# Kernel optimization log

Measured on AMD Instinct MI355X. Metric: run time of the kernel, lower is better.

The kernel has to match this reference:

```python
import jax, jax.numpy as jnp
import numpy as np

B, S, D, H = 2, 2048, 1024, 16
DK = D // H


def setup_inputs() -> dict:
    key = jax.random.key(0)
    ks = jax.random.split(key, 12)
    init = lambda k, shp: (jax.random.normal(k, shp, dtype=jnp.float32) * 0.02)
    return {
        'query': jax.random.normal(ks[0], (B, S, D), dtype=jnp.float32),
        'key_in': jax.random.normal(ks[1], (B, S, D), dtype=jnp.float32),
        'value': jax.random.normal(ks[2], (B, S, D), dtype=jnp.float32),
        'w_q': init(ks[3], (D, D)), 'b_q': jnp.zeros((D,), jnp.float32),
        'w_k': init(ks[4], (D, D)), 'b_k': jnp.zeros((D,), jnp.float32),
        'w_v': init(ks[5], (D, D)), 'b_v': jnp.zeros((D,), jnp.float32),
        'w_o': init(ks[6], (D, D)), 'b_o': jnp.zeros((D,), jnp.float32),
        'fuzzy_centers': jax.random.normal(ks[7], (H, 3), dtype=jnp.float32),
        'fuzzy_widths': jnp.ones((H, 3), jnp.float32),
        'temperature': jnp.ones((1,), jnp.float32),
    }


def reference(query, key_in, value, w_q, b_q, w_k, b_k, w_v, b_v, w_o, b_o,
              fuzzy_centers, fuzzy_widths, temperature):
    b, s, d = query.shape
    h, dk = H, DK
    proj = lambda x, w, bias: x @ w.T + bias
    # [b,s,d] -> [b,h,s,dk]
    Q = proj(query, w_q, b_q).reshape(b, s, h, dk).transpose(0, 2, 1, 3)
    K = proj(key_in, w_k, b_k).reshape(b, s, h, dk).transpose(0, 2, 1, 3)
    V = proj(value, w_v, b_v).reshape(b, s, h, dk).transpose(0, 2, 1, 3)
    scores = jnp.einsum('bhsd,bhtd->bhst', Q, K) / np.sqrt(dk).astype(np.float32)
    # Faithful to torch: every (head,func) gaussian is applied to ALL heads' scores,
    # so each score gets sum of h*3 memberships, divided by 3.
    c = fuzzy_centers.reshape(-1)
    w = fuzzy_widths.reshape(-1)
    fz = jnp.zeros_like(scores)
    for i in range(h * 3):  # small fixed loop over membership functions
        fz = fz + jnp.exp(-(scores - c[i]) ** 2 / (2.0 * w[i] ** 2))
    fz = (fz / 3.0) / temperature[0]
    attn = jax.nn.softmax(fz, axis=-1)
    attended = jnp.einsum('bhst,bhtd->bhsd', attn, V)
    attended = attended.transpose(0, 2, 1, 3).reshape(b, s, d)
    return attended @ w_o.T + b_o
```

## Files before the change

### kernel.cpp

```cpp
#include <hip/hip_runtime.h>
#include <hip/hip_bf16.h>


#define S_LEN 2048
#define DMODEL 1024
#define NHEAD 16
#define DKH 64
#define NLUT 2048
#define LUT_MIN (-10.0f)
#define LUT_MAX (10.0f)

typedef __attribute__((ext_vector_type(8))) short bfx8;
typedef __attribute__((ext_vector_type(4))) float fx4;
typedef __attribute__((ext_vector_type(16))) float fx16;
typedef __attribute__((ext_vector_type(4))) unsigned ux4;

__device__ __forceinline__ short f2bf(float x) {
    unsigned u = __builtin_bit_cast(unsigned, x);
    u = (u + 0x7fffu + ((u >> 16) & 1u)) >> 16;
    return (short)u;
}

__device__ __forceinline__ unsigned cvt_pk_bf16(float lo, float hi) {
    unsigned r;
    asm("v_cvt_pk_bf16_f32 %0, %1, %2" : "=v"(r) : "v"(lo), "v"(hi));
    return r;
}

__device__ __forceinline__ void plane_swap(unsigned& a, unsigned& b) {
    asm volatile("v_permlane32_swap_b32 %0, %1" : "+v"(a), "+v"(b));
}

__device__ __forceinline__ void stage8_f32(const float* __restrict__ src, short* dst) {
    float4 a = *(const float4*)(src);
    float4 b = *(const float4*)(src + 4);
    bfx8 r;
    r[0] = f2bf(a.x); r[1] = f2bf(a.y); r[2] = f2bf(a.z); r[3] = f2bf(a.w);
    r[4] = f2bf(b.x); r[5] = f2bf(b.y); r[6] = f2bf(b.z); r[7] = f2bf(b.w);
    *(bfx8*)dst = r;
}

__device__ __forceinline__ void gload_lds16(const void* g, void* l) {
    __builtin_amdgcn_global_load_lds(
        (const __attribute__((address_space(1))) unsigned int*)g,
        (__attribute__((address_space(3))) unsigned int*)l, 16, 0, 0);
}

__device__ void lut_body(const float* __restrict__ centers, const float* __restrict__ widths,
                         const float* __restrict__ temp, float2* __restrict__ lutf) {
    __shared__ float fzb[NLUT];
    __shared__ float red[256];
    __shared__ float cs[48], wsb[48];
    int tid = threadIdx.x;
    if (tid < 48) { cs[tid] = centers[tid]; wsb[tid] = widths[tid]; }
    __syncthreads();
    float invT = 1.0f / temp[0];
    const float step = (LUT_MAX - LUT_MIN) / (float)(NLUT - 1);
    float lmax = -1e30f;
    for (int i = tid; i < NLUT; i += 256) {
        float s = LUT_MIN + step * (float)i;
        float fz = 0.0f;
        #pragma unroll 1
        for (int j = 0; j < 48; j++) {
            float d = s - cs[j];
            float w = wsb[j];
            fz += expf(-(d * d) / (2.0f * w * w));
        }
        fz = fz * (1.0f / 3.0f) * invT;
        fzb[i] = fz;
        lmax = fmaxf(lmax, fz);
    }
    red[tid] = lmax;
    __syncthreads();
    for (int off = 128; off > 0; off >>= 1) {
        if (tid < off) red[tid] = fmaxf(red[tid], red[tid + off]);
        __syncthreads();
    }
    float m = red[0];
    __syncthreads();
    for (int i = tid; i < NLUT; i += 256) fzb[i] = expf(fzb[i] - m);
    __syncthreads();
    for (int i = tid; i < NLUT; i += 256) {
        float g0 = fzb[i];
        float g1 = fzb[(i + 1 < NLUT) ? i + 1 : NLUT - 1];
        lutf[i] = make_float2(g0, g1 - g0);
    }
}

__global__ void build_lut_pk(const float* centers, const float* widths,
                             const float* temp, float2* lutf) {
    lut_body(centers, widths, temp, lutf);
}

__global__ void cast_bf16(const float* __restrict__ src, short* __restrict__ dst, int n8) {
    int i = blockIdx.x * 256 + threadIdx.x;
    if (i < n8) stage8_f32(src + (size_t)i * 8, dst + (size_t)i * 8);
}

__global__ void prep_all(const float* q, const float* kin, const float* v,
        const float* wq, const float* wk, const float* wv, const float* wo,
        short* xq, short* xk, short* xv,
        short* bwq, short* bwk, short* bwv, short* bwo,
        const float* centers, const float* widths, const float* temp,
        float2* lutf) {
    int bid = blockIdx.x;
    if (bid >= 8192) {
        lut_body(centers, widths, temp, lutf);
        return;
    }
    const float* src; short* dst; int blk;
    if (bid < 6144) {
        int y = bid >> 11; blk = bid & 2047;
        src = (y == 0) ? q : (y == 1) ? kin : v;
        dst = (y == 0) ? xq : (y == 1) ? xk : xv;
    } else {
        int y = (bid - 6144) >> 9; blk = (bid - 6144) & 511;
        src = (y == 0) ? wq : (y == 1) ? wk : (y == 2) ? wv : wo;
        dst = (y == 0) ? bwq : (y == 1) ? bwk : (y == 2) ? bwv : bwo;
    }
    size_t i = (size_t)blk * 256 + threadIdx.x;
    stage8_f32(src + i * 8, (short*)dst + i * 8);
}

struct GemmJob {
    const short* A; const short* W; const float* bias;
    short* obf; float* of32; int mode; float scale;
};

__global__ __launch_bounds__(256, 3) void gemm128(GemmJob j0, GemmJob j1, GemmJob j2) {
    __shared__ __align__(16) short As[2][128 * 32];
    __shared__ __align__(16) short Bs[2][128 * 32];
    GemmJob jb = (blockIdx.z == 0) ? j0 : (blockIdx.z == 1) ? j1 : j2;
    int tid = threadIdx.x, wave = tid >> 6, lane = tid & 63, quad = lane >> 4, l15 = lane & 15;
    int m0 = blockIdx.y * 128, n0 = blockIdx.x * 128;
    int wm = (wave >> 1) * 64, wn = (wave & 1) * 64;

    fx4 acc[4][4];
    #pragma unroll
    for (int i = 0; i < 4; i++)
        #pragma unroll
        for (int j = 0; j < 4; j++)
            #pragma unroll
            for (int r = 0; r < 4; r++) acc[i][j][r] = 0.0f;

    int fc = (quad ^ ((l15 >> 1) & 3)) * 8;

    int srow[2], sgc[2];
    #pragma unroll
    for (int r = 0; r < 2; r++) {
        int slot = r * 256 + wave * 64 + lane;
        srow[r] = slot >> 2;
        sgc[r] = (slot & 3) ^ ((srow[r] >> 1) & 3);
    }

    auto stage = [&](int k0, int buf) {
        #pragma unroll
        for (int r = 0; r < 2; r++) {
            gload_lds16(jb.A + (size_t)(m0 + srow[r]) * DMODEL + k0 + sgc[r] * 8,
                        &As[buf][(r * 256 + wave * 64) * 8]);
            gload_lds16(jb.W + (size_t)(n0 + srow[r]) * DMODEL + k0 + sgc[r] * 8,
                        &Bs[buf][(r * 256 + wave * 64) * 8]);
        }
    };

    stage(0, 0);
    __syncthreads();
    int buf = 0;
    for (int k0 = 0; k0 < DMODEL; k0 += 32) {
        if (k0 + 32 < DMODEL) stage(k0 + 32, buf ^ 1);
        bfx8 af[4], bfr[4];
        #pragma unroll
        for (int i = 0; i < 4; i++) af[i] = *(const bfx8*)(&As[buf][(wm + i * 16 + l15) * 32 + fc]);
        #pragma unroll
        for (int j = 0; j < 4; j++) bfr[j] = *(const bfx8*)(&Bs[buf][(wn + j * 16 + l15) * 32 + fc]);
        #pragma unroll
        for (int i = 0; i < 4; i++)
            #pragma unroll
            for (int j = 0; j < 4; j++)
                acc[i][j] = __builtin_amdgcn_mfma_f32_16x16x32_bf16(af[i], bfr[j], acc[i][j], 0, 0, 0);
        __syncthreads();
        buf ^= 1;
    }

    #pragma unroll
    for (int j = 0; j < 4; j++) {
        int n = n0 + wn + j * 16 + l15;
        float bv = jb.bias[n];
        #pragma unroll
        for (int i = 0; i < 4; i++) {
            #pragma unroll
            for (int r = 0; r < 4; r++) {
                int m = m0 + wm + i * 16 + quad * 4 + r;
                float v = (acc[i][j][r] + bv) * jb.scale;
                if (jb.mode == 0) {
                    int b = m >> 11, s = m & 2047, h = n >> 6, dk = n & 63;
                    jb.obf[(((size_t)(b * NHEAD + h)) * S_LEN + s) * DKH + dk] = f2bf(v);
                } else if (jb.mode == 1) {
                    int b = m >> 11, s = m & 2047, h = n >> 6, dk = n & 63;
                    jb.obf[(((size_t)(b * NHEAD + h)) * DKH + dk) * S_LEN + s] = f2bf(v);
                } else {
                    jb.of32[(size_t)m * DMODEL + n] = v;
                }
            }
        }
    }
}

__global__ __launch_bounds__(256, 4) void flash_fuzzy(const short* __restrict__ Qb,
        const short* __restrict__ Kb, const short* __restrict__ VTb,
        const float2* __restrict__ lutg, short* __restrict__ AO) {
    __shared__ __align__(16) short Ks[64 * 64];
    __shared__ __align__(16) short Vs[64 * 64];
    __shared__ __align__(16) float2 lutf[NLUT];

    int tid = threadIdx.x, wave = tid >> 6, lane = tid & 63;
    int l31 = lane & 31, hi = lane >> 5;
    int wq = wave >> 1, st = wave & 1;
    int q0 = blockIdx.x * 64, bh = blockIdx.y;
    const short* Qp = Qb + (size_t)bh * S_LEN * DKH;
    const short* Kp = Kb + (size_t)bh * S_LEN * DKH;
    const short* Vp = VTb + (size_t)bh * DKH * S_LEN;

    #pragma unroll
    for (int i = tid; i < NLUT / 2; i += 256)
        ((float4*)lutf)[i] = ((const float4*)lutg)[i];

    bfx8 aq[4];
    #pragma unroll
    for (int ks = 0; ks < 4; ks++)
        aq[ks] = *(const bfx8*)(Qp + (size_t)(q0 + wq * 32 + l31) * DKH + ks * 16 + hi * 8);

    bfx8 ones;
    #pragma unroll
    for (int i = 0; i < 8; i++) ones[i] = (short)0x3F80;

    fx16 oacc[2];
    fx16 dacc;
    #pragma unroll
    for (int r = 0; r < 16; r++) dacc[r] = 0.0f;
    #pragma unroll
    for (int dt = 0; dt < 2; dt++)
        #pragma unroll
        for (int r = 0; r < 16; r++) oacc[dt][r] = 0.0f;

    const float invh = (float)(NLUT - 1) / (LUT_MAX - LUT_MIN);
    const float xoff = -LUT_MIN * invh;

    int srow[2], sgc[2];
    #pragma unroll
    for (int r = 0; r < 2; r++) {
        int slot = (wave * 2 + r) * 64 + lane;
        srow[r] = slot >> 3;
        sgc[r] = (slot & 7) ^ (srow[r] & 7);
    }

    for (int t0 = 0; t0 < S_LEN; t0 += 64) {
        __syncthreads();
        #pragma unroll
        for (int r = 0; r < 2; r++) {
            gload_lds16(Kp + (size_t)(t0 + srow[r]) * DKH + sgc[r] * 8,
                        &Ks[((wave * 2 + r) * 64) * 8]);
            gload_lds16(Vp + (size_t)srow[r] * S_LEN + t0 + sgc[r] * 8,
                        &Vs[((wave * 2 + r) * 64) * 8]);
        }
        __syncthreads();

        fx16 sac;
        #pragma unroll
        for (int r = 0; r < 16; r++) sac[r] = 0.0f;
        {
            int row = st * 32 + l31;
            #pragma unroll
            for (int ks = 0; ks < 4; ks++) {
                bfx8 kf = *(const bfx8*)(&Ks[row * 64 + (((ks * 2 + hi) ^ (row & 7)) * 8)]);
                sac = __builtin_amdgcn_mfma_f32_32x32x16_bf16(kf, aq[ks], sac, 0, 0, 0);
            }
        }

        unsigned w[8];
        #pragma unroll
        for (int t = 0; t < 8; t++) {
            float pv[2];
            #pragma unroll
            for (int u = 0; u < 2; u++) {
                float s = sac[t * 2 + u];
                float x = fmaf(s, invh, xoff);
                x = __builtin_amdgcn_fmed3f(x, 0.0f, (float)(NLUT - 1));
                int j = (int)x;
                float f = x - floorf(x);
                float2 pr = lutf[j];
                pv[u] = fmaf(f, pr.y, pr.x);
            }
            w[t] = cvt_pk_bf16(pv[0], pv[1]);
        }

        plane_swap(w[0], w[2]); plane_swap(w[1], w[3]);
        plane_swap(w[4], w[6]); plane_swap(w[5], w[7]);
        ux4 b0v = {w[0], w[1], w[2], w[3]};
        ux4 b1v = {w[4], w[5], w[6], w[7]};
        bfx8 pb0 = __builtin_bit_cast(bfx8, b0v);
        bfx8 pb1 = __builtin_bit_cast(bfx8, b1v);

        #pragma unroll
        for (int dt = 0; dt < 2; dt++) {
            int row = dt * 32 + l31;
            bfx8 v0f = *(const bfx8*)(&Vs[row * 64 + (((st * 4 + 0 + hi) ^ (row & 7)) * 8)]);
            bfx8 v1f = *(const bfx8*)(&Vs[row * 64 + (((st * 4 + 2 + hi) ^ (row & 7)) * 8)]);
            oacc[dt] = __builtin_amdgcn_mfma_f32_32x32x16_bf16(v0f, pb0, oacc[dt], 0, 0, 0);
            oacc[dt] = __builtin_amdgcn_mfma_f32_32x32x16_bf16(v1f, pb1, oacc[dt], 0, 0, 0);
        }
        dacc = __builtin_amdgcn_mfma_f32_32x32x16_bf16(ones, pb0, dacc, 0, 0, 0);
        dacc = __builtin_amdgcn_mfma_f32_32x32x16_bf16(ones, pb1, dacc, 0, 0, 0);
    }

    float den = dacc[0];

    __syncthreads();
    float* obuf = (wq == 0) ? (float*)Ks : (float*)Vs;
    float* dbuf = (float*)lutf;
    if (st == 1) {
        #pragma unroll
        for (int dt = 0; dt < 2; dt++)
            #pragma unroll
            for (int r = 0; r < 16; r++)
                obuf[(dt * 16 + r) * 64 + lane] = oacc[dt][r];
        dbuf[wq * 64 + lane] = den;
    }
    __syncthreads();
    if (st == 0) {
        float dtot = den + dbuf[wq * 64 + lane];
        int b = bh >> 4, h = bh & 15;
        #pragma unroll
        for (int dt = 0; dt < 2; dt++) {
            #pragma unroll
            for (int r = 0; r < 16; r++) {
                float o = oacc[dt][r] + obuf[(dt * 16 + r) * 64 + lane];
                int dk = dt * 32 + (r & 3) + 8 * (r >> 2) + 4 * hi;
                int q = q0 + wq * 32 + l31;
                AO[((size_t)(b * S_LEN + q)) * DMODEL + h * DKH + dk] = f2bf(o / dtot);
            }
        }
    }
}

extern "C" void kernel_launch(void* const* d_in, const int* in_sizes, int n_in,
                              void* d_out, int out_size, void* d_ws, size_t ws_size,
                              hipStream_t stream) {
    const float* query   = (const float*)d_in[0];
    const float* key_in  = (const float*)d_in[1];
    const float* value   = (const float*)d_in[2];
    const float* w_q     = (const float*)d_in[3];
    const float* b_q     = (const float*)d_in[4];
    const float* w_k     = (const float*)d_in[5];
    const float* b_k     = (const float*)d_in[6];
    const float* w_v     = (const float*)d_in[7];
    const float* b_v     = (const float*)d_in[8];
    const float* w_o     = (const float*)d_in[9];
    const float* b_o     = (const float*)d_in[10];
    const float* centers = (const float*)d_in[11];
    const float* widths  = (const float*)d_in[12];
    const float* temp    = (const float*)d_in[13];

    char* p = (char*)d_ws;
    auto alloc = [&](size_t bytes) -> void* {
        void* r = (void*)p;
        p += (bytes + 255) & ~(size_t)255;
        return r;
    };
    const size_t nBHSD = (size_t)2 * NHEAD * S_LEN * DKH;
    const size_t nW    = (size_t)DMODEL * DMODEL;
    float2* lutp = (float2*)alloc(NLUT * 8);
    short* Qb  = (short*)alloc(nBHSD * 2);
    short* Kb  = (short*)alloc(nBHSD * 2);
    short* VTb = (short*)alloc(nBHSD * 2);

    char* save = p;
    short* xq  = (short*)alloc(nBHSD * 2);
    short* xk  = (short*)alloc(nBHSD * 2);
    short* xv  = (short*)alloc(nBHSD * 2);
    short* bwq = (short*)alloc(nW * 2);
    short* bwk = (short*)alloc(nW * 2);
    short* bwv = (short*)alloc(nW * 2);
    short* bwo = (short*)alloc(nW * 2);
    bool fused = ((size_t)(p - (char*)d_ws) <= ws_size);

    dim3 blk(256);
    dim3 gq(8, 32, 3), g1(8, 32, 1), fg(32, 32);
    GemmJob JO;

    if (fused) {
        short* AO = xq;
        prep_all<<<dim3(8193), blk, 0, stream>>>(query, key_in, value, w_q, w_k, w_v, w_o,
                xq, xk, xv, bwq, bwk, bwv, bwo, centers, widths, temp, lutp);
        GemmJob JQ = {xq, bwq, b_q, Qb,  nullptr, 0, 0.125f};
        GemmJob JK = {xk, bwk, b_k, Kb,  nullptr, 0, 1.0f};
        GemmJob JV = {xv, bwv, b_v, VTb, nullptr, 1, 1.0f};
        gemm128<<<gq, blk, 0, stream>>>(JQ, JK, JV);
        flash_fuzzy<<<fg, blk, 0, stream>>>(Qb, Kb, VTb, lutp, AO);
        JO = {AO, bwo, b_o, nullptr, (float*)d_out, 2, 1.0f};
        gemm128<<<g1, blk, 0, stream>>>(JO, JO, JO);
    } else {
        p = save;
        short* xf = (short*)alloc(nBHSD * 2);
        short* wb = (short*)alloc(nW * 2);
        short* AO = xf;
        const int n8x = (int)(nBHSD / 8), n8w = (int)(nW / 8);
        dim3 cg((n8x + 255) / 256), cw((n8w + 255) / 256);
        build_lut_pk<<<dim3(1), blk, 0, stream>>>(centers, widths, temp, lutp);
        cast_bf16<<<cg, blk, 0, stream>>>(query, xf, n8x);
        cast_bf16<<<cw, blk, 0, stream>>>(w_q, wb, n8w);
        JO = {xf, wb, b_q, Qb, nullptr, 0, 0.125f};
        gemm128<<<g1, blk, 0, stream>>>(JO, JO, JO);
        cast_bf16<<<cg, blk, 0, stream>>>(key_in, xf, n8x);
        cast_bf16<<<cw, blk, 0, stream>>>(w_k, wb, n8w);
        JO = {xf, wb, b_k, Kb, nullptr, 0, 1.0f};
        gemm128<<<g1, blk, 0, stream>>>(JO, JO, JO);
        cast_bf16<<<cg, blk, 0, stream>>>(value, xf, n8x);
        cast_bf16<<<cw, blk, 0, stream>>>(w_v, wb, n8w);
        JO = {xf, wb, b_v, VTb, nullptr, 1, 1.0f};
        gemm128<<<g1, blk, 0, stream>>>(JO, JO, JO);
        flash_fuzzy<<<fg, blk, 0, stream>>>(Qb, Kb, VTb, lutp, AO);
        cast_bf16<<<cw, blk, 0, stream>>>(w_o, wb, n8w);
        JO = {AO, wb, b_o, nullptr, (float*)d_out, 2, 1.0f};
        gemm128<<<g1, blk, 0, stream>>>(JO, JO, JO);
    }
}
```

Measured before the change: 301.1 us.

## Parallelize LUT build, pack LUT as bf16 pairs, read V directly from global

Builds the softmax LUT across 8 blocks using a fixed upper bound instead of a block-wide max reduction, and stores it as packed bf16 pairs rather than float2. This halves the LUT's LDS footprint. The flash kernel drops the V shared-memory tile and loads V fragments straight from global memory. It also changes the K swizzle and makes prep_all grid-stride over 1024 blocks. The intent is to remove the serial single-block LUT tail and to cut LDS use for better occupancy. The costs are lower LUT precision (bf16), possible overflow or underflow from the fixed bound, and uncoalesced or redundant global V reads.

```diff
diff --git a/kernel.cpp b/kernel.cpp
--- a/kernel.cpp
+++ b/kernel.cpp
@@ -46,50 +46,44 @@
         (__attribute__((address_space(3))) unsigned int*)l, 16, 0, 0);
 }
 
-__device__ void lut_body(const float* __restrict__ centers, const float* __restrict__ widths,
-                         const float* __restrict__ temp, float2* __restrict__ lutf) {
-    __shared__ float fzb[NLUT];
-    __shared__ float red[256];
-    __shared__ float cs[48], wsb[48];
+__device__ void lut_slice(const float* __restrict__ centers, const float* __restrict__ widths,
+                          const float* __restrict__ temp, unsigned* __restrict__ lutp,
+                          int slice) {
+    __shared__ float cs[48], iw[48];
+    __shared__ float gsh[257];
     int tid = threadIdx.x;
-    if (tid < 48) { cs[tid] = centers[tid]; wsb[tid] = widths[tid]; }
+    if (tid < 48) {
+        cs[tid] = centers[tid];
+        float w = widths[tid];
+        iw[tid] = -0.5f / (w * w);
+    }
     __syncthreads();
     float invT = 1.0f / temp[0];
     const float step = (LUT_MAX - LUT_MIN) / (float)(NLUT - 1);
-    float lmax = -1e30f;
-    for (int i = tid; i < NLUT; i += 256) {
+    float bound = 16.0f * invT;
+    int base = slice * 256;
+    #pragma unroll 1
+    for (int idx = tid; idx < 257; idx += 256) {
+        int i = base + idx; if (i > NLUT - 1) i = NLUT - 1;
         float s = LUT_MIN + step * (float)i;
-        float fz = 0.0f;
-        #pragma unroll 1
+        float a = 0.0f;
+        #pragma unroll
         for (int j = 0; j < 48; j++) {
             float d = s - cs[j];
-            float w = wsb[j];
-            fz += expf(-(d * d) / (2.0f * w * w));
-        }
-        fz = fz * (1.0f / 3.0f) * invT;
-        fzb[i] = fz;
-        lmax = fmaxf(lmax, fz);
-    }
-    red[tid] = lmax;
+            a += expf(d * d * iw[j]);
+        }
+        float fz = a * (1.0f / 3.0f) * invT;
+        gsh[idx] = expf(fz - bound);
+    }
     __syncthreads();
-    for (int off = 128; off > 0; off >>= 1) {
-        if (tid < off) red[tid] = fmaxf(red[tid], red[tid + off]);
-        __syncthreads();
-    }
-    float m = red[0];
-    __syncthreads();
-    for (int i = tid; i < NLUT; i += 256) fzb[i] = expf(fzb[i] - m);
-    __syncthreads();
-    for (int i = tid; i < NLUT; i += 256) {
-        float g0 = fzb[i];
-        float g1 = fzb[(i + 1 < NLUT) ? i + 1 : NLUT - 1];
-        lutf[i] = make_float2(g0, g1 - g0);
-    }
+    unsigned lo = (unsigned short)f2bf(gsh[tid]);
+    unsigned hi = (unsigned short)f2bf(gsh[tid + 1]);
+    lutp[base + tid] = lo | (hi << 16);
 }
 
 __global__ void build_lut_pk(const float* centers, const float* widths,
-                             const float* temp, float2* lutf) {
-    lut_body(centers, widths, temp, lutf);
+                             const float* temp, unsigned* lutp) {
+    lut_slice(centers, widths, temp, lutp, blockIdx.x);
 }
 
 __global__ void cast_bf16(const float* __restrict__ src, short* __restrict__ dst, int n8) {
@@ -102,24 +96,26 @@
         short* xq, short* xk, short* xv,
         short* bwq, short* bwk, short* bwv, short* bwo,
         const float* centers, const float* widths, const float* temp,
-        float2* lutf) {
+        unsigned* lutp) {
     int bid = blockIdx.x;
-    if (bid >= 8192) {
-        lut_body(centers, widths, temp, lutf);
+    if (bid >= 1024) {
+        lut_slice(centers, widths, temp, lutp, bid - 1024);
         return;
     }
-    const float* src; short* dst; int blk;
-    if (bid < 6144) {
-        int y = bid >> 11; blk = bid & 2047;
-        src = (y == 0) ? q : (y == 1) ? kin : v;
-        dst = (y == 0) ? xq : (y == 1) ? xk : xv;
-    } else {
-        int y = (bid - 6144) >> 9; blk = (bid - 6144) & 511;
-        src = (y == 0) ? wq : (y == 1) ? wk : (y == 2) ? wv : wo;
-        dst = (y == 0) ? bwq : (y == 1) ? bwk : (y == 2) ? bwv : bwo;
-    }
-    size_t i = (size_t)blk * 256 + threadIdx.x;
-    stage8_f32(src + i * 8, (short*)dst + i * 8);
+    for (int vb = bid; vb < 8192; vb += 1024) {
+        const float* src; short* dst; int blk;
+        if (vb < 6144) {
+            int y = vb >> 11; blk = vb & 2047;
+            src = (y == 0) ? q : (y == 1) ? kin : v;
+            dst = (y == 0) ? xq : (y == 1) ? xk : xv;
+        } else {
+            int y = (vb - 6144) >> 9; blk = (vb - 6144) & 511;
+            src = (y == 0) ? wq : (y == 1) ? wk : (y == 2) ? wv : wo;
+            dst = (y == 0) ? bwq : (y == 1) ? bwk : (y == 2) ? bwv : bwo;
+        }
+        size_t i = (size_t)blk * 256 + threadIdx.x;
+        stage8_f32(src + i * 8, (short*)dst + i * 8);
+    }
 }
 
 struct GemmJob {
@@ -208,10 +204,10 @@
 
 __global__ __launch_bounds__(256, 4) void flash_fuzzy(const short* __restrict__ Qb,
         const short* __restrict__ Kb, const short* __restrict__ VTb,
-        const float2* __restrict__ lutg, short* __restrict__ AO) {
+        const unsigned* __restrict__ lutg, short* __restrict__ AO) {
     __shared__ __align__(16) short Ks[64 * 64];
-    __shared__ __align__(16) short Vs[64 * 64];
-    __shared__ __align__(16) float2 lutf[NLUT];
+    __shared__ unsigned lut[NLUT];
+    __shared__ float dbuf[128];
 
     int tid = threadIdx.x, wave = tid >> 6, lane = tid & 63;
     int l31 = lane & 31, hi = lane >> 5;
@@ -222,8 +218,8 @@
     const short* Vp = VTb + (size_t)bh * DKH * S_LEN;
 
     #pragma unroll
-    for (int i = tid; i < NLUT / 2; i += 256)
-        ((float4*)lutf)[i] = ((const float4*)lutg)[i];
+    for (int i = tid; i < NLUT / 4; i += 256)
+        ((uint4*)lut)[i] = ((const uint4*)lutg)[i];
 
     bfx8 aq[4];
     #pragma unroll
@@ -251,30 +247,33 @@
     for (int r = 0; r < 2; r++) {
         int slot = (wave * 2 + r) * 64 + lane;
         srow[r] = slot >> 3;
-        sgc[r] = (slot & 7) ^ (srow[r] & 7);
-    }
+        sgc[r] = (slot & 7) ^ ((srow[r] ^ (srow[r] >> 3)) & 7);
+    }
+
+    int krow = st * 32 + l31;
+    int kphi = (krow ^ (krow >> 3)) & 7;
+    const short* vbase = Vp + (size_t)l31 * S_LEN + st * 32 + hi * 8;
 
     for (int t0 = 0; t0 < S_LEN; t0 += 64) {
         __syncthreads();
         #pragma unroll
-        for (int r = 0; r < 2; r++) {
+        for (int r = 0; r < 2; r++)
             gload_lds16(Kp + (size_t)(t0 + srow[r]) * DKH + sgc[r] * 8,
                         &Ks[((wave * 2 + r) * 64) * 8]);
-            gload_lds16(Vp + (size_t)srow[r] * S_LEN + t0 + sgc[r] * 8,
-                        &Vs[((wave * 2 + r) * 64) * 8]);
-        }
         __syncthreads();
 
+        bfx8 vr00 = *(const bfx8*)(vbase + t0);
+        bfx8 vr01 = *(const bfx8*)(vbase + t0 + 16);
+        bfx8 vr10 = *(const bfx8*)(vbase + (size_t)32 * S_LEN + t0);
+        bfx8 vr11 = *(const bfx8*)(vbase + (size_t)32 * S_LEN + t0 + 16);
+
         fx16 sac;
         #pragma unroll
         for (int r = 0; r < 16; r++) sac[r] = 0.0f;
-        {
-            int row = st * 32 + l31;
-            #pragma unroll
-            for (int ks = 0; ks < 4; ks++) {
-                bfx8 kf = *(const bfx8*)(&Ks[row * 64 + (((ks * 2 + hi) ^ (row & 7)) * 8)]);
-                sac = __builtin_amdgcn_mfma_f32_32x32x16_bf16(kf, aq[ks], sac, 0, 0, 0);
-            }
+        #pragma unroll
+        for (int ks = 0; ks < 4; ks++) {
+            bfx8 kf = *(const bfx8*)(&Ks[krow * 64 + (((ks * 2 + hi) ^ kphi) * 8)]);
+            sac = __builtin_amdgcn_mfma_f32_32x32x16_bf16(kf, aq[ks], sac, 0, 0, 0);
         }
 
         unsigned w[8];
@@ -287,9 +286,11 @@
                 float x = fmaf(s, invh, xoff);
                 x = __builtin_amdgcn_fmed3f(x, 0.0f, (float)(NLUT - 1));
                 int j = (int)x;
-                float f = x - floorf(x);
-                float2 pr = lutf[j];
-                pv[u] = fmaf(f, pr.y, pr.x);
+                float f = x - (float)j;
+                unsigned pr = lut[j];
+                float v0 = __builtin_bit_cast(float, pr << 16);
+                float v1 = __builtin_bit_cast(float, pr & 0xffff0000u);
+                pv[u] = fmaf(f, v1 - v0, v0);
             }
             w[t] = cvt_pk_bf16(pv[0], pv[1]);
         }
@@ -301,14 +302,10 @@
         bfx8 pb0 = __builtin_bit_cast(bfx8, b0v);
         bfx8 pb1 = __builtin_bit_cast(bfx8, b1v);
 
-        #pragma unroll
-        for (int dt = 0; dt < 2; dt++) {
-            int row = dt * 32 + l31;
-            bfx8 v0f = *(const bfx8*)(&Vs[row * 64 + (((st * 4 + 0 + hi) ^ (row & 7)) * 8)]);
-            bfx8 v1f = *(const bfx8*)(&Vs[row * 64 + (((st * 4 + 2 + hi) ^ (row & 7)) * 8)]);
-            oacc[dt] = __builtin_amdgcn_mfma_f32_32x32x16_bf16(v0f, pb0, oacc[dt], 0, 0, 0);
-            oacc[dt] = __builtin_amdgcn_mfma_f32_32x32x16_bf16(v1f, pb1, oacc[dt], 0, 0, 0);
-        }
+        oacc[0] = __builtin_amdgcn_mfma_f32_32x32x16_bf16(vr00, pb0, oacc[0], 0, 0, 0);
+        oacc[0] = __builtin_amdgcn_mfma_f32_32x32x16_bf16(vr01, pb1, oacc[0], 0, 0, 0);
+        oacc[1] = __builtin_amdgcn_mfma_f32_32x32x16_bf16(vr10, pb0, oacc[1], 0, 0, 0);
+        oacc[1] = __builtin_amdgcn_mfma_f32_32x32x16_bf16(vr11, pb1, oacc[1], 0, 0, 0);
         dacc = __builtin_amdgcn_mfma_f32_32x32x16_bf16(ones, pb0, dacc, 0, 0, 0);
         dacc = __builtin_amdgcn_mfma_f32_32x32x16_bf16(ones, pb1, dacc, 0, 0, 0);
     }
@@ -316,8 +313,7 @@
     float den = dacc[0];
 
     __syncthreads();
-    float* obuf = (wq == 0) ? (float*)Ks : (float*)Vs;
-    float* dbuf = (float*)lutf;
+    float* obuf = (wq == 0) ? (float*)Ks : (float*)lut;
     if (st == 1) {
         #pragma unroll
         for (int dt = 0; dt < 2; dt++)
@@ -369,7 +365,7 @@
     };
     const size_t nBHSD = (size_t)2 * NHEAD * S_LEN * DKH;
     const size_t nW    = (size_t)DMODEL * DMODEL;
-    float2* lutp = (float2*)alloc(NLUT * 8);
+    unsigned* lutp = (unsigned*)alloc(NLUT * 4);
     short* Qb  = (short*)alloc(nBHSD * 2);
     short* Kb  = (short*)alloc(nBHSD * 2);
     short* VTb = (short*)alloc(nBHSD * 2);
@@ -390,7 +386,7 @@
 
     if (fused) {
         short* AO = xq;
-        prep_all<<<dim3(8193), blk, 0, stream>>>(query, key_in, value, w_q, w_k, w_v, w_o,
+        prep_all<<<dim3(1032), blk, 0, stream>>>(query, key_in, value, w_q, w_k, w_v, w_o,
                 xq, xk, xv, bwq, bwk, bwv, bwo, centers, widths, temp, lutp);
         GemmJob JQ = {xq, bwq, b_q, Qb,  nullptr, 0, 0.125f};
         GemmJob JK = {xk, bwk, b_k, Kb,  nullptr, 0, 1.0f};
@@ -406,7 +402,7 @@
         short* AO = xf;
         const int n8x = (int)(nBHSD / 8), n8w = (int)(nW / 8);
         dim3 cg((n8x + 255) / 256), cw((n8w + 255) / 256);
-        build_lut_pk<<<dim3(1), blk, 0, stream>>>(centers, widths, temp, lutp);
+        build_lut_pk<<<dim3(8), blk, 0, stream>>>(centers, widths, temp, lutp);
         cast_bf16<<<cg, blk, 0, stream>>>(query, xf, n8x);
         cast_bf16<<<cw, blk, 0, stream>>>(w_q, wb, n8w);
         JO = {xf, wb, b_q, Qb, nullptr, 0, 0.125f};
```

Measured after the change: 277.2 us. 8.0% less time.
